# Performance work log

Hardware: AMD Instinct MI355X
Metric: run time of the kernel (lower is better)

Reference implementation:

```python
import jax, jax.numpy as jnp
import numpy as np

B, T, C = 4, 1024, 1024
H, D = 16, 64


def setup_inputs() -> dict:
    key = jax.random.key(0)
    ks = jax.random.split(key, 5)
    sc = 0.02
    x = jax.random.normal(ks[0], (B, T, C), dtype=jnp.float32)
    Wq = jax.random.normal(ks[1], (H, C, D), dtype=jnp.float32) * sc
    Wk = jax.random.normal(ks[2], (H, C, D), dtype=jnp.float32) * sc
    Wv = jax.random.normal(ks[3], (H, C, D), dtype=jnp.float32) * sc
    Wp = jax.random.normal(ks[4], (H * D, C), dtype=jnp.float32) * sc
    bp = jnp.zeros((C,), dtype=jnp.float32)
    return {"x": x, "Wq": Wq, "Wk": Wk, "Wv": Wv, "Wp": Wp, "bp": bp}


def reference(x, Wq, Wk, Wv, Wp, bp):
    # per-head projections (bias-free, as in nanoGPT Head)
    q = jnp.einsum('btc,hcd->bhtd', x, Wq)
    k = jnp.einsum('btc,hcd->bhtd', x, Wk)
    v = jnp.einsum('btc,hcd->bhtd', x, Wv)
    scale = 1.0 / jnp.sqrt(jnp.asarray(D, dtype=x.dtype))
    scores = jnp.einsum('bhtd,bhsd->bhts', q, k) * scale  # [B,H,T,T]
    causal = jnp.tril(jnp.ones((T, T), dtype=bool))
    scores = jnp.where(causal, scores, jnp.asarray(-jnp.inf, dtype=scores.dtype))
    attn = jax.nn.softmax(scores, axis=-1)
    out = jnp.einsum('bhts,bhsd->bhtd', attn, v)  # [B,H,T,D]
    out = out.transpose(0, 2, 1, 3).reshape(B, T, H * D)  # concat heads
    return out @ Wp + bp  # final projection (dropout=0)
```

## Files before the change

kernel.cpp:

```cpp
#include <hip/hip_runtime.h>
#include <hip/hip_bf16.h>

typedef unsigned short u16;
typedef __bf16 bf16x8 __attribute__((ext_vector_type(8)));
typedef float floatx4 __attribute__((ext_vector_type(4)));

#define SB 4
#define ST 1024
#define SC 1024
#define SH 16
#define SD 64

__device__ __forceinline__ u16 f2bf(float f) {
    unsigned int u = __builtin_bit_cast(unsigned int, f);
    u += 0x7fffu + ((u >> 16) & 1u);
    return (u16)(u >> 16);
}

__device__ __forceinline__ void gload16(const u16* g, u16* l) {
    __builtin_amdgcn_global_load_lds(
        (const __attribute__((address_space(1))) unsigned int*)g,
        (__attribute__((address_space(3))) unsigned int*)l, 16, 0, 0);
}

__global__ void k_prep(const float* __restrict__ x,
                       const float* __restrict__ Wq, const float* __restrict__ Wk,
                       const float* __restrict__ Wv, const float* __restrict__ Wp,
                       u16* __restrict__ xb, u16* __restrict__ Wqkv, u16* __restrict__ Wpt) {
    __shared__ float tile[64 * 65];
    const int id = blockIdx.x, tid = threadIdx.x;
    if (id < 4096) {
        int i = id * 256 + tid;
        float4 v = ((const float4*)x)[i];
        uint2 o;
        o.x = (unsigned)f2bf(v.x) | ((unsigned)f2bf(v.y) << 16);
        o.y = (unsigned)f2bf(v.z) | ((unsigned)f2bf(v.w) << 16);
        ((uint2*)xb)[i] = o;
    } else if (id < 4864) {
        const int id1 = id - 4096;
        const int qkv = id1 >> 8, rem = id1 & 255, h = rem >> 4, c0 = (rem & 15) * 64;
        const float* src = qkv == 0 ? Wq : (qkv == 1 ? Wk : Wv);
        #pragma unroll
        for (int i = 0; i < 16; ++i) {
            int idx = tid + i * 256;
            int r = idx >> 6, d = idx & 63;
            tile[r * 65 + d] = src[(h * SC + c0 + r) * SD + d];
        }
        __syncthreads();
        #pragma unroll
        for (int i = 0; i < 16; ++i) {
            int idx = tid + i * 256;
            int d = idx >> 6, cc = idx & 63;
            Wqkv[(qkv * 1024 + h * SD + d) * SC + c0 + cc] = f2bf(tile[cc * 65 + d]);
        }
    } else {
        const int id2 = id - 4864;
        const int n0 = (id2 & 15) * 64, k0 = (id2 >> 4) * 64;
        #pragma unroll
        for (int i = 0; i < 16; ++i) {
            int idx = tid + i * 256;
            int r = idx >> 6, nn = idx & 63;
            tile[r * 65 + nn] = Wp[(k0 + r) * SC + n0 + nn];
        }
        __syncthreads();
        #pragma unroll
        for (int i = 0; i < 16; ++i) {
            int idx = tid + i * 256;
            int nr = idx >> 6, kk = idx & 63;
            Wpt[(n0 + nr) * (SH * SD) + k0 + kk] = f2bf(tile[kk * 65 + nr]);
        }
    }
}

__launch_bounds__(256)
__global__ void k_gemm(const u16* __restrict__ A, const u16* __restrict__ Bt,
                       int M, int N, int K,
                       u16* __restrict__ Qb, u16* __restrict__ Kb, u16* __restrict__ Vt) {
    constexpr int BM = 128, BN = 128, SM = 4, SN = 4;
    __shared__ u16 Als[2][BM * 64];
    __shared__ u16 Bls[2][BN * 64];
    const int tid = threadIdx.x, lane = tid & 63, w = tid >> 6;
    const int quad = lane >> 4, l16 = lane & 15;
    const int sr = lane >> 3, sc = lane & 7;
    const int nt = N / BN;
    const int m0 = (blockIdx.x / nt) * BM, n0 = (blockIdx.x % nt) * BN;
    const int wm = (w >> 1) * 64, wn = (w & 1) * 64;

    auto stage = [&](int buf, int k0) {
        #pragma unroll
        for (int i = 0; i < 4; ++i) {
            int rb = (w * 4 + i) * 8;
            gload16(&A[(long)(m0 + rb + sr) * K + k0 + ((sc ^ sr) << 3)], &Als[buf][rb * 64]);
            gload16(&Bt[(long)(n0 + rb + sr) * K + k0 + ((sc ^ sr) << 3)], &Bls[buf][rb * 64]);
        }
    };

    floatx4 acc[SM][SN] = {};
    const int niter = K / 64;
    stage(0, 0);
    for (int it = 0; it < niter; ++it) {
        const int buf = it & 1;
        __syncthreads();
        if (it + 1 < niter) stage(buf ^ 1, (it + 1) * 64);
        bf16x8 af[SM][2], bfr[SN][2];
        #pragma unroll
        for (int sm = 0; sm < SM; ++sm) {
            int row = wm + sm * 16 + l16;
            #pragma unroll
            for (int ks = 0; ks < 2; ++ks)
                af[sm][ks] = *(const bf16x8*)&Als[buf][row * 64 + (((ks * 4 + quad) ^ (row & 7)) << 3)];
        }
        #pragma unroll
        for (int sn = 0; sn < SN; ++sn) {
            int row = wn + sn * 16 + l16;
            #pragma unroll
            for (int ks = 0; ks < 2; ++ks)
                bfr[sn][ks] = *(const bf16x8*)&Bls[buf][row * 64 + (((ks * 4 + quad) ^ (row & 7)) << 3)];
        }
        #pragma unroll
        for (int ks = 0; ks < 2; ++ks)
            #pragma unroll
            for (int sm = 0; sm < SM; ++sm)
                #pragma unroll
                for (int sn = 0; sn < SN; ++sn)
                    acc[sm][sn] = __builtin_amdgcn_mfma_f32_16x16x32_bf16(bfr[sn][ks], af[sm][ks], acc[sm][sn], 0, 0, 0);
    }
    const int qkv = n0 >> 10;
    const float qs = qkv == 0 ? 0.18033688011112042f : 1.0f;
    #pragma unroll
    for (int sm = 0; sm < SM; ++sm) {
        const int m = m0 + wm + sm * 16 + l16;
        const int bb = m >> 10, t = m & 1023;
        #pragma unroll
        for (int sn = 0; sn < SN; ++sn) {
            const int dl = (n0 & 1023) + wn + sn * 16 + (quad << 2);
            const int h = dl >> 6, d0 = dl & 63;
            u16 pk[4];
            #pragma unroll
            for (int r = 0; r < 4; ++r) pk[r] = f2bf(acc[sm][sn][r] * qs);
            if (qkv == 2) {
                const long vb = (long)(bb * SH + h) * SD * ST + t;
                #pragma unroll
                for (int r = 0; r < 4; ++r) Vt[vb + (long)(d0 + r) * ST] = pk[r];
            } else {
                u16* dst = qkv == 0 ? Qb : Kb;
                *(uint2*)&dst[(((long)(bb * SH + h) * ST + t) << 6) + d0] = *(uint2*)pk;
            }
        }
    }
}

__launch_bounds__(256)
__global__ void k_oproj(const u16* __restrict__ A, const u16* __restrict__ Bt,
                        const float* __restrict__ bias, float* __restrict__ Cout) {
    constexpr int K = 1024, N = 1024, BM = 128, SM = 4, SN = 4;
    __shared__ u16 Als[2][BM * 64];
    __shared__ u16 Bls[2][128 * 64];
    const int tid = threadIdx.x, lane = tid & 63, w = tid >> 6;
    const int quad = lane >> 4, l16 = lane & 15;
    const int sr = lane >> 3, sc = lane & 7;
    const int m0 = (blockIdx.x >> 3) * BM, n0 = (blockIdx.x & 7) * 128;
    const int wm = (w >> 1) * 64, wn = (w & 1) * 64;

    auto stage = [&](int buf, int k0) {
        #pragma unroll
        for (int i = 0; i < 4; ++i) {
            int rb = (w * 4 + i) * 8;
            gload16(&A[(long)(m0 + rb + sr) * K + k0 + ((sc ^ sr) << 3)], &Als[buf][rb * 64]);
            gload16(&Bt[(long)(n0 + rb + sr) * K + k0 + ((sc ^ sr) << 3)], &Bls[buf][rb * 64]);
        }
    };

    floatx4 acc[SM][SN] = {};
    const int niter = K / 64;
    stage(0, 0);
    for (int it = 0; it < niter; ++it) {
        const int buf = it & 1;
        __syncthreads();
        if (it + 1 < niter) stage(buf ^ 1, (it + 1) * 64);
        bf16x8 af[SM][2], bfr[SN][2];
        #pragma unroll
        for (int sm = 0; sm < SM; ++sm) {
            int row = wm + sm * 16 + l16;
            #pragma unroll
            for (int ks = 0; ks < 2; ++ks)
                af[sm][ks] = *(const bf16x8*)&Als[buf][row * 64 + (((ks * 4 + quad) ^ (row & 7)) << 3)];
        }
        #pragma unroll
        for (int sn = 0; sn < SN; ++sn) {
            int row = wn + sn * 16 + l16;
            #pragma unroll
            for (int ks = 0; ks < 2; ++ks)
                bfr[sn][ks] = *(const bf16x8*)&Bls[buf][row * 64 + (((ks * 4 + quad) ^ (row & 7)) << 3)];
        }
        #pragma unroll
        for (int ks = 0; ks < 2; ++ks)
            #pragma unroll
            for (int sm = 0; sm < SM; ++sm)
                #pragma unroll
                for (int sn = 0; sn < SN; ++sn)
                    acc[sm][sn] = __builtin_amdgcn_mfma_f32_16x16x32_bf16(bfr[sn][ks], af[sm][ks], acc[sm][sn], 0, 0, 0);
    }
    #pragma unroll
    for (int sn = 0; sn < SN; ++sn) {
        const int nb = n0 + wn + sn * 16 + (quad << 2);
        const float4 bv = *(const float4*)&bias[nb];
        #pragma unroll
        for (int sm = 0; sm < SM; ++sm) {
            const int m = m0 + wm + sm * 16 + l16;
            float4 o;
            o.x = acc[sm][sn][0] + bv.x;
            o.y = acc[sm][sn][1] + bv.y;
            o.z = acc[sm][sn][2] + bv.z;
            o.w = acc[sm][sn][3] + bv.w;
            *(float4*)&Cout[(long)m * N + nb] = o;
        }
    }
}

__launch_bounds__(256)
__global__ void k_attn(const u16* __restrict__ Qg, const u16* __restrict__ Kg,
                       const u16* __restrict__ Vtg, u16* __restrict__ Og) {
    __shared__ u16 Kls[2][64 * 64];
    __shared__ u16 Vls[2][64 * 64];
    __shared__ u16 Pls[64 * 64];
    const int tid = threadIdx.x, lane = tid & 63, w = tid >> 6;
    const int quad = lane >> 4, l16 = lane & 15;
    const int sr = lane >> 3, sc = lane & 7;
    const int tile = 15 - (blockIdx.x >> 6);
    const int bh = blockIdx.x & 63;
    const int t0 = tile * 64;
    const int b = bh >> 4, h = bh & 15;
    const u16* Qbh = Qg + (long)bh * ST * SD;
    const u16* Kbh = Kg + (long)bh * ST * SD;
    const u16* Vbh = Vtg + (long)bh * SD * ST;

    bf16x8 qf[2];
    {
        const u16* qrow = Qbh + (t0 + w * 16 + l16) * SD;
        qf[0] = *(const bf16x8*)&qrow[quad * 8];
        qf[1] = *(const bf16x8*)&qrow[32 + quad * 8];
    }
    floatx4 oacc[4] = {};
    float lsum = 0.f;
    const int myt = t0 + w * 16 + l16;
    const int rowP = w * 16 + l16;

    auto stage = [&](int buf, int s0) {
        #pragma unroll
        for (int i = 0; i < 2; ++i) {
            int rb = (w * 2 + i) * 8;
            gload16(&Kbh[(s0 + rb + sr) * SD + ((sc ^ sr) << 3)], &Kls[buf][rb * 64]);
            gload16(&Vbh[(rb + sr) * ST + s0 + ((sc ^ sr) << 3)], &Vls[buf][rb * 64]);
        }
    };

    stage(0, 0);
    for (int j = 0; j <= tile; ++j) {
        const int buf = j & 1;
        const int s0 = j * 64;
        __syncthreads();
        if (j < tile) stage(buf ^ 1, s0 + 64);

        floatx4 sa[4] = {};
        #pragma unroll
        for (int sn = 0; sn < 4; ++sn) {
            int row = sn * 16 + l16;
            #pragma unroll
            for (int ks = 0; ks < 2; ++ks) {
                bf16x8 kf = *(const bf16x8*)&Kls[buf][row * 64 + (((ks * 4 + quad) ^ (row & 7)) << 3)];
                sa[sn] = __builtin_amdgcn_mfma_f32_16x16x32_bf16(kf, qf[ks], sa[sn], 0, 0, 0);
            }
        }
        const bool diag = (j == tile);
        #pragma unroll
        for (int sn = 0; sn < 4; ++sn) {
            const int sl = sn * 16 + (quad << 2);
            u16 pk[4];
            #pragma unroll
            for (int r = 0; r < 4; ++r) {
                float e = __builtin_exp2f(sa[sn][r]);
                if (diag && s0 + sl + r > myt) e = 0.f;
                lsum += e;
                pk[r] = (u16)(__builtin_bit_cast(unsigned int, e) >> 16);
            }
            *(uint2*)&Pls[rowP * 64 + (((sl >> 3) ^ (rowP & 7)) << 3) + ((quad & 1) << 2)] = *(uint2*)pk;
        }
        bf16x8 pf[2];
        #pragma unroll
        for (int ks = 0; ks < 2; ++ks)
            pf[ks] = *(const bf16x8*)&Pls[rowP * 64 + (((ks * 4 + quad) ^ (rowP & 7)) << 3)];
        #pragma unroll
        for (int dn = 0; dn < 4; ++dn) {
            int row = dn * 16 + l16;
            #pragma unroll
            for (int ks = 0; ks < 2; ++ks) {
                bf16x8 vf = *(const bf16x8*)&Vls[buf][row * 64 + (((ks * 4 + quad) ^ (row & 7)) << 3)];
                oacc[dn] = __builtin_amdgcn_mfma_f32_16x16x32_bf16(vf, pf[ks], oacc[dn], 0, 0, 0);
            }
        }
    }
    float l = lsum;
    l += __shfl_xor(l, 16);
    l += __shfl_xor(l, 32);
    const float inv = 1.0f / l;
    const long obase = ((long)(b * ST + myt) << 10) + h * SD;
    #pragma unroll
    for (int dn = 0; dn < 4; ++dn) {
        u16 pk[4];
        #pragma unroll
        for (int r = 0; r < 4; ++r) pk[r] = f2bf(oacc[dn][r] * inv);
        *(uint2*)&Og[obase + dn * 16 + (quad << 2)] = *(uint2*)pk;
    }
}

extern "C" void kernel_launch(void* const* d_in, const int* in_sizes, int n_in,
                              void* d_out, int out_size, void* d_ws, size_t ws_size,
                              hipStream_t stream) {
    const float* x  = (const float*)d_in[0];
    const float* Wq = (const float*)d_in[1];
    const float* Wk = (const float*)d_in[2];
    const float* Wv = (const float*)d_in[3];
    const float* Wp = (const float*)d_in[4];
    const float* bp = (const float*)d_in[5];
    float* out = (float*)d_out;

    char* ws = (char*)d_ws;
    u16* xb   = (u16*)(ws);
    u16* Wqkv = (u16*)(ws + (8ll  << 20));
    u16* Wpt  = (u16*)(ws + (14ll << 20));
    u16* Qb   = (u16*)(ws + (16ll << 20));
    u16* Kb   = (u16*)(ws + (24ll << 20));
    u16* Vt   = (u16*)(ws + (32ll << 20));
    u16* Ob   = (u16*)(ws + (40ll << 20));

    k_prep<<<5120, 256, 0, stream>>>(x, Wq, Wk, Wv, Wp, xb, Wqkv, Wpt);
    k_gemm<<<32 * 24, 256, 0, stream>>>(xb, Wqkv, 4096, 3072, 1024, Qb, Kb, Vt);
    k_attn<<<1024, 256, 0, stream>>>(Qb, Kb, Vt, Ob);
    k_oproj<<<256, 256, 0, stream>>>(Ob, Wpt, bp, out);
}
```

Before: 170.6 us.

## Retile QKV and output GEMMs, process two query tiles per attention block

The QKV GEMM now uses 128x96 tiles (1024 blocks) and the output projection uses 128x64 tiles (512 blocks), giving more blocks to fill the GPU's CUs. The epilogue now computes the q/k/v selector per column slice, because a 96-wide tile can straddle the q/k boundary. Attention blocks each handle 128 query rows as two 64-row halves that share every staged K/V tile, which halves K/V traffic per query. Blocks are ordered in paired heavy/light causal tiles. The cost is a causal-mask compare on every tile plus more registers and LDS per attention block, which may reduce occupancy.

```diff
diff --git a/kernel.cpp b/kernel.cpp
--- a/kernel.cpp
+++ b/kernel.cpp
@@ -74,34 +74,35 @@
 
 __launch_bounds__(256)
 __global__ void k_gemm(const u16* __restrict__ A, const u16* __restrict__ Bt,
-                       int M, int N, int K,
                        u16* __restrict__ Qb, u16* __restrict__ Kb, u16* __restrict__ Vt) {
-    constexpr int BM = 128, BN = 128, SM = 4, SN = 4;
+    constexpr int K = 1024, BM = 128, BN = 96, SM = 4, SN = 3;
     __shared__ u16 Als[2][BM * 64];
     __shared__ u16 Bls[2][BN * 64];
     const int tid = threadIdx.x, lane = tid & 63, w = tid >> 6;
     const int quad = lane >> 4, l16 = lane & 15;
     const int sr = lane >> 3, sc = lane & 7;
-    const int nt = N / BN;
-    const int m0 = (blockIdx.x / nt) * BM, n0 = (blockIdx.x % nt) * BN;
-    const int wm = (w >> 1) * 64, wn = (w & 1) * 64;
+    const int m0 = (blockIdx.x >> 5) * BM, n0 = (blockIdx.x & 31) * BN;
+    const int wm = (w >> 1) * 64, wn = (w & 1) * 48;
 
     auto stage = [&](int buf, int k0) {
         #pragma unroll
         for (int i = 0; i < 4; ++i) {
             int rb = (w * 4 + i) * 8;
             gload16(&A[(long)(m0 + rb + sr) * K + k0 + ((sc ^ sr) << 3)], &Als[buf][rb * 64]);
+        }
+        #pragma unroll
+        for (int i = 0; i < 3; ++i) {
+            int rb = (w * 3 + i) * 8;
             gload16(&Bt[(long)(n0 + rb + sr) * K + k0 + ((sc ^ sr) << 3)], &Bls[buf][rb * 64]);
         }
     };
 
     floatx4 acc[SM][SN] = {};
-    const int niter = K / 64;
     stage(0, 0);
-    for (int it = 0; it < niter; ++it) {
+    for (int it = 0; it < 16; ++it) {
         const int buf = it & 1;
         __syncthreads();
-        if (it + 1 < niter) stage(buf ^ 1, (it + 1) * 64);
+        if (it < 15) stage(buf ^ 1, (it + 1) * 64);
         bf16x8 af[SM][2], bfr[SN][2];
         #pragma unroll
         for (int sm = 0; sm < SM; ++sm) {
@@ -125,16 +126,17 @@
                 for (int sn = 0; sn < SN; ++sn)
                     acc[sm][sn] = __builtin_amdgcn_mfma_f32_16x16x32_bf16(bfr[sn][ks], af[sm][ks], acc[sm][sn], 0, 0, 0);
     }
-    const int qkv = n0 >> 10;
-    const float qs = qkv == 0 ? 0.18033688011112042f : 1.0f;
     #pragma unroll
-    for (int sm = 0; sm < SM; ++sm) {
-        const int m = m0 + wm + sm * 16 + l16;
-        const int bb = m >> 10, t = m & 1023;
-        #pragma unroll
-        for (int sn = 0; sn < SN; ++sn) {
-            const int dl = (n0 & 1023) + wn + sn * 16 + (quad << 2);
-            const int h = dl >> 6, d0 = dl & 63;
+    for (int sn = 0; sn < SN; ++sn) {
+        const int c0 = n0 + wn + sn * 16;
+        const int qkv = c0 >> 10;
+        const float qs = qkv == 0 ? 0.18033688011112042f : 1.0f;
+        const int cs = (c0 & 1023) + (quad << 2);
+        const int h = cs >> 6, d0 = cs & 63;
+        #pragma unroll
+        for (int sm = 0; sm < SM; ++sm) {
+            const int m = m0 + wm + sm * 16 + l16;
+            const int bb = m >> 10, t = m & 1023;
             u16 pk[4];
             #pragma unroll
             for (int r = 0; r < 4; ++r) pk[r] = f2bf(acc[sm][sn][r] * qs);
@@ -153,31 +155,34 @@
 __launch_bounds__(256)
 __global__ void k_oproj(const u16* __restrict__ A, const u16* __restrict__ Bt,
                         const float* __restrict__ bias, float* __restrict__ Cout) {
-    constexpr int K = 1024, N = 1024, BM = 128, SM = 4, SN = 4;
+    constexpr int K = 1024, N = 1024, BM = 128, BN = 64, SM = 4, SN = 2;
     __shared__ u16 Als[2][BM * 64];
-    __shared__ u16 Bls[2][128 * 64];
+    __shared__ u16 Bls[2][BN * 64];
     const int tid = threadIdx.x, lane = tid & 63, w = tid >> 6;
     const int quad = lane >> 4, l16 = lane & 15;
     const int sr = lane >> 3, sc = lane & 7;
-    const int m0 = (blockIdx.x >> 3) * BM, n0 = (blockIdx.x & 7) * 128;
-    const int wm = (w >> 1) * 64, wn = (w & 1) * 64;
+    const int m0 = (blockIdx.x >> 4) * BM, n0 = (blockIdx.x & 15) * BN;
+    const int wm = (w >> 1) * 64, wn = (w & 1) * 32;
 
     auto stage = [&](int buf, int k0) {
         #pragma unroll
         for (int i = 0; i < 4; ++i) {
             int rb = (w * 4 + i) * 8;
             gload16(&A[(long)(m0 + rb + sr) * K + k0 + ((sc ^ sr) << 3)], &Als[buf][rb * 64]);
+        }
+        #pragma unroll
+        for (int i = 0; i < 2; ++i) {
+            int rb = (w * 2 + i) * 8;
             gload16(&Bt[(long)(n0 + rb + sr) * K + k0 + ((sc ^ sr) << 3)], &Bls[buf][rb * 64]);
         }
     };
 
     floatx4 acc[SM][SN] = {};
-    const int niter = K / 64;
     stage(0, 0);
-    for (int it = 0; it < niter; ++it) {
+    for (int it = 0; it < 16; ++it) {
         const int buf = it & 1;
         __syncthreads();
-        if (it + 1 < niter) stage(buf ^ 1, (it + 1) * 64);
+        if (it < 15) stage(buf ^ 1, (it + 1) * 64);
         bf16x8 af[SM][2], bfr[SN][2];
         #pragma unroll
         for (int sm = 0; sm < SM; ++sm) {
@@ -223,27 +228,28 @@
                        const u16* __restrict__ Vtg, u16* __restrict__ Og) {
     __shared__ u16 Kls[2][64 * 64];
     __shared__ u16 Vls[2][64 * 64];
-    __shared__ u16 Pls[64 * 64];
+    __shared__ u16 Pls[128 * 64];
     const int tid = threadIdx.x, lane = tid & 63, w = tid >> 6;
     const int quad = lane >> 4, l16 = lane & 15;
     const int sr = lane >> 3, sc = lane & 7;
-    const int tile = 15 - (blockIdx.x >> 6);
+    const int g = blockIdx.x >> 6;
+    const int qt = (g < 4) ? (7 - g) : (g - 4);
     const int bh = blockIdx.x & 63;
-    const int t0 = tile * 64;
+    const int t0 = qt * 128;
     const int b = bh >> 4, h = bh & 15;
     const u16* Qbh = Qg + (long)bh * ST * SD;
     const u16* Kbh = Kg + (long)bh * ST * SD;
     const u16* Vbh = Vtg + (long)bh * SD * ST;
 
-    bf16x8 qf[2];
-    {
-        const u16* qrow = Qbh + (t0 + w * 16 + l16) * SD;
-        qf[0] = *(const bf16x8*)&qrow[quad * 8];
-        qf[1] = *(const bf16x8*)&qrow[32 + quad * 8];
-    }
-    floatx4 oacc[4] = {};
-    float lsum = 0.f;
-    const int myt = t0 + w * 16 + l16;
+    bf16x8 qf[2][2];
+    #pragma unroll
+    for (int half = 0; half < 2; ++half) {
+        const u16* qrow = Qbh + (t0 + half * 64 + w * 16 + l16) * SD;
+        qf[half][0] = *(const bf16x8*)&qrow[quad * 8];
+        qf[half][1] = *(const bf16x8*)&qrow[32 + quad * 8];
+    }
+    floatx4 oacc[2][4] = {};
+    float lsum[2] = {0.f, 0.f};
     const int rowP = w * 16 + l16;
 
     auto stage = [&](int buf, int s0) {
@@ -255,62 +261,77 @@
         }
     };
 
+    const int jmax = 2 * qt + 1;
     stage(0, 0);
-    for (int j = 0; j <= tile; ++j) {
+    for (int j = 0; j <= jmax; ++j) {
         const int buf = j & 1;
         const int s0 = j * 64;
         __syncthreads();
-        if (j < tile) stage(buf ^ 1, s0 + 64);
-
-        floatx4 sa[4] = {};
+        if (j < jmax) stage(buf ^ 1, s0 + 64);
+
+        floatx4 sa[2][4] = {};
         #pragma unroll
         for (int sn = 0; sn < 4; ++sn) {
             int row = sn * 16 + l16;
             #pragma unroll
             for (int ks = 0; ks < 2; ++ks) {
                 bf16x8 kf = *(const bf16x8*)&Kls[buf][row * 64 + (((ks * 4 + quad) ^ (row & 7)) << 3)];
-                sa[sn] = __builtin_amdgcn_mfma_f32_16x16x32_bf16(kf, qf[ks], sa[sn], 0, 0, 0);
+                sa[0][sn] = __builtin_amdgcn_mfma_f32_16x16x32_bf16(kf, qf[0][ks], sa[0][sn], 0, 0, 0);
+                sa[1][sn] = __builtin_amdgcn_mfma_f32_16x16x32_bf16(kf, qf[1][ks], sa[1][sn], 0, 0, 0);
             }
         }
-        const bool diag = (j == tile);
-        #pragma unroll
-        for (int sn = 0; sn < 4; ++sn) {
-            const int sl = sn * 16 + (quad << 2);
-            u16 pk[4];
-            #pragma unroll
-            for (int r = 0; r < 4; ++r) {
-                float e = __builtin_exp2f(sa[sn][r]);
-                if (diag && s0 + sl + r > myt) e = 0.f;
-                lsum += e;
-                pk[r] = (u16)(__builtin_bit_cast(unsigned int, e) >> 16);
+        #pragma unroll
+        for (int half = 0; half < 2; ++half) {
+            const int myt_h = t0 + half * 64 + w * 16 + l16;
+            const int rp = half * 64 + rowP;
+            #pragma unroll
+            for (int sn = 0; sn < 4; ++sn) {
+                const int sl = sn * 16 + (quad << 2);
+                u16 pk[4];
+                #pragma unroll
+                for (int r = 0; r < 4; ++r) {
+                    float e = __builtin_exp2f(sa[half][sn][r]);
+                    if (s0 + sl + r > myt_h) e = 0.f;
+                    lsum[half] += e;
+                    pk[r] = (u16)(__builtin_bit_cast(unsigned int, e) >> 16);
+                }
+                *(uint2*)&Pls[rp * 64 + (((sl >> 3) ^ (rp & 7)) << 3) + ((quad & 1) << 2)] = *(uint2*)pk;
             }
-            *(uint2*)&Pls[rowP * 64 + (((sl >> 3) ^ (rowP & 7)) << 3) + ((quad & 1) << 2)] = *(uint2*)pk;
-        }
-        bf16x8 pf[2];
-        #pragma unroll
-        for (int ks = 0; ks < 2; ++ks)
-            pf[ks] = *(const bf16x8*)&Pls[rowP * 64 + (((ks * 4 + quad) ^ (rowP & 7)) << 3)];
+        }
+        bf16x8 pf[2][2];
+        #pragma unroll
+        for (int half = 0; half < 2; ++half) {
+            const int rp = half * 64 + rowP;
+            #pragma unroll
+            for (int ks = 0; ks < 2; ++ks)
+                pf[half][ks] = *(const bf16x8*)&Pls[rp * 64 + (((ks * 4 + quad) ^ (rp & 7)) << 3)];
+        }
         #pragma unroll
         for (int dn = 0; dn < 4; ++dn) {
             int row = dn * 16 + l16;
             #pragma unroll
             for (int ks = 0; ks < 2; ++ks) {
                 bf16x8 vf = *(const bf16x8*)&Vls[buf][row * 64 + (((ks * 4 + quad) ^ (row & 7)) << 3)];
-                oacc[dn] = __builtin_amdgcn_mfma_f32_16x16x32_bf16(vf, pf[ks], oacc[dn], 0, 0, 0);
+                oacc[0][dn] = __builtin_amdgcn_mfma_f32_16x16x32_bf16(vf, pf[0][ks], oacc[0][dn], 0, 0, 0);
+                oacc[1][dn] = __builtin_amdgcn_mfma_f32_16x16x32_bf16(vf, pf[1][ks], oacc[1][dn], 0, 0, 0);
             }
         }
     }
-    float l = lsum;
-    l += __shfl_xor(l, 16);
-    l += __shfl_xor(l, 32);
-    const float inv = 1.0f / l;
-    const long obase = ((long)(b * ST + myt) << 10) + h * SD;
     #pragma unroll
-    for (int dn = 0; dn < 4; ++dn) {
-        u16 pk[4];
-        #pragma unroll
-        for (int r = 0; r < 4; ++r) pk[r] = f2bf(oacc[dn][r] * inv);
-        *(uint2*)&Og[obase + dn * 16 + (quad << 2)] = *(uint2*)pk;
+    for (int half = 0; half < 2; ++half) {
+        float l = lsum[half];
+        l += __shfl_xor(l, 16);
+        l += __shfl_xor(l, 32);
+        const float inv = 1.0f / l;
+        const int myt_h = t0 + half * 64 + w * 16 + l16;
+        const long obase = ((long)(b * ST + myt_h) << 10) + h * SD;
+        #pragma unroll
+        for (int dn = 0; dn < 4; ++dn) {
+            u16 pk[4];
+            #pragma unroll
+            for (int r = 0; r < 4; ++r) pk[r] = f2bf(oacc[half][dn][r] * inv);
+            *(uint2*)&Og[obase + dn * 16 + (quad << 2)] = *(uint2*)pk;
+        }
     }
 }
 
@@ -335,7 +356,7 @@
     u16* Ob   = (u16*)(ws + (40ll << 20));
 
     k_prep<<<5120, 256, 0, stream>>>(x, Wq, Wk, Wv, Wp, xb, Wqkv, Wpt);
-    k_gemm<<<32 * 24, 256, 0, stream>>>(xb, Wqkv, 4096, 3072, 1024, Qb, Kb, Vt);
-    k_attn<<<1024, 256, 0, stream>>>(Qb, Kb, Vt, Ob);
-    k_oproj<<<256, 256, 0, stream>>>(Ob, Wpt, bp, out);
-}
+    k_gemm<<<1024, 256, 0, stream>>>(xb, Wqkv, Qb, Kb, Vt);
+    k_attn<<<512, 256, 0, stream>>>(Qb, Kb, Vt, Ob);
+    k_oproj<<<512, 256, 0, stream>>>(Ob, Wpt, bp, out);
+}
```

Result: no change. 172.2 us (+0.9%).
